# Kernel tuning notes

Hardware: AMD Instinct MI355X
Metric: run time of the kernel (lower is better)

Reference implementation:

```python
import math
import jax, jax.numpy as jnp
from jax import lax
import numpy as np

B, SEQ, D_MODEL = 8, 1024, 512
R, K, H = 3, 3, 4
DE, DH, DU, DTR, DCONV, DEMB = 64, 64, 32, 4, 3, 10


def setup_inputs() -> dict:
    key = jax.random.key(0)
    ks = iter(jax.random.split(key, 48))
    def nrm(shape, s=0.05):
        return jax.random.normal(next(ks), shape, jnp.float32) * s
    inp = {}
    inp['x'] = jax.random.normal(next(ks), (B, SEQ, D_MODEL), jnp.float32)
    # Mamba params, leading dims (R, 2) = (layer, fwd/bwd direction)
    inp['m_in_w'] = nrm((R, 2, D_MODEL, 2 * DE))
    inp['m_conv_w'] = nrm((R, 2, DE, DCONV), 0.2)
    inp['m_conv_b'] = nrm((R, 2, DE), 0.1)
    inp['m_xproj_w'] = nrm((R, 2, DE, DTR + 2 * DH))
    inp['m_dt_w'] = nrm((R, 2, DTR, DE), 0.2)
    inp['m_dt_b'] = nrm((R, 2, DE), 0.1)
    inp['m_Alog'] = jnp.broadcast_to(jnp.log(jnp.arange(1, DH + 1, dtype=jnp.float32)), (R, 2, DE, DH)) + jnp.zeros((R, 2, DE, DH), jnp.float32)
    inp['m_D'] = jnp.ones((R, 2, DE), jnp.float32)
    inp['m_out_w'] = nrm((R, 2, DE, D_MODEL))
    # LayerNorm / FFN params per layer
    inp['ln1_g'] = jnp.ones((R, D_MODEL), jnp.float32)
    inp['ln1_b'] = jnp.zeros((R, D_MODEL), jnp.float32)
    inp['ffn_w1'] = nrm((R, D_MODEL, DU))
    inp['ffn_b1'] = jnp.zeros((R, DU), jnp.float32)
    inp['ffn_w2'] = nrm((R, DU, D_MODEL))
    inp['ffn_b2'] = jnp.zeros((R, D_MODEL), jnp.float32)
    inp['ln2_g'] = jnp.ones((R, D_MODEL), jnp.float32)
    inp['ln2_b'] = jnp.zeros((R, D_MODEL), jnp.float32)
    # MAGAC params (N = D_MODEL nodes, in_dim = SEQ)
    inp['psi_emb'] = jax.random.normal(next(ks), (D_MODEL, DEMB), jnp.float32)
    inp['psi'] = jnp.array(1.0, jnp.float32)
    inp['W_q'] = jax.random.normal(next(ks), (DEMB, H, DEMB), jnp.float32)
    inp['W_k'] = jax.random.normal(next(ks), (DEMB, H, DEMB), jnp.float32)
    inp['attn_alpha'] = jnp.array(0.5, jnp.float32)
    inp['F_w'] = nrm((H, DEMB, K + 1, SEQ))
    inp['f_b'] = jax.random.normal(next(ks), (H, DEMB), jnp.float32)
    inp['head_mix'] = jnp.ones((H,), jnp.float32)
    inp['head_w'] = nrm((D_MODEL,))
    inp['head_b'] = jnp.zeros((), jnp.float32)
    return inp


def _layernorm(x, g, b, eps=1e-5):
    mu = x.mean(-1, keepdims=True)
    v = ((x - mu) ** 2).mean(-1, keepdims=True)
    return (x - mu) / jnp.sqrt(v + eps) * g + b


def _mamba(x, in_w, conv_w, conv_b, xproj_w, dt_w, dt_b, Alog, Dp, out_w):
    b, l, _ = x.shape
    xr = x @ in_w                              # (b,l,2*DE)
    xp, res = jnp.split(xr, 2, axis=-1)
    # depthwise causal conv (torch pads k-1 both sides then truncates to l == left-pad k-1)
    xc = xp.transpose(0, 2, 1)                 # (b,DE,l)
    xc = lax.conv_general_dilated(xc, conv_w[:, None, :], (1,), [(DCONV - 1, 0)],
                                  feature_group_count=DE,
                                  dimension_numbers=('NCH', 'OIH', 'NCH'))
    xc = xc + conv_b[None, :, None]
    xp = jax.nn.silu(xc.transpose(0, 2, 1))    # (b,l,DE)
    A = -jnp.exp(Alog)                         # (DE,DH)
    x_dbl = xp @ xproj_w                       # (b,l,DTR+2*DH)
    delta = jax.nn.softplus(x_dbl[..., :DTR] @ dt_w + dt_b)   # (b,l,DE)
    Bm = x_dbl[..., DTR:DTR + DH]
    Cm = x_dbl[..., DTR + DH:]
    dA = jnp.exp(delta[..., None] * A)                         # (b,l,DE,DH)
    dBu = delta[..., None] * Bm[:, :, None, :] * xp[..., None] # (b,l,DE,DH)
    def step(s, inp):
        dAt, dBt, ct = inp
        s = dAt * s + dBt
        return s, jnp.einsum('bdn,bn->bd', s, ct)
    s0 = jnp.zeros((b, DE, DH), x.dtype)
    _, ys = lax.scan(step, s0, (dA.transpose(1, 0, 2, 3), dBu.transpose(1, 0, 2, 3), Cm.transpose(1, 0, 2)))
    y = ys.transpose(1, 0, 2) + xp * Dp
    y = y * jax.nn.sigmoid(res)
    return y @ out_w


def _magac(xg, psi_emb, psi, W_q, W_k, attn_alpha, F_w, f_b, head_mix):
    # xg: (B, N, L); eval-mode deterministic path
    diff = psi_emb[:, None, :] - psi_emb[None, :, :]
    A_base = jax.nn.softmax(jnp.exp(-psi * (diff ** 2).sum(-1)), axis=1)   # (N,N)
    Q = jnp.einsum('nd,dhm->nhm', psi_emb, W_q)
    Kq = jnp.einsum('nd,dhm->nhm', psi_emb, W_k)
    attn = jax.nn.softmax(jnp.einsum('nhd,mhd->hnm', Q, Kq) / math.sqrt(DEMB), axis=-1)
    alpha = jax.nn.sigmoid(attn_alpha)
    A_eff = alpha * A_base[None] + (1.0 - alpha) * attn                    # (H,N,N)
    N = psi_emb.shape[0]
    I = jnp.broadcast_to(jnp.eye(N, dtype=xg.dtype), (H, N, N))
    sup = [I, A_eff]
    for _ in range(K - 1):
        sup.append(2.0 * jnp.matmul(A_eff, sup[-1]) - sup[-2])             # Chebyshev
    sup = jnp.stack(sup, axis=1)                                           # (H,K+1,N,N)
    Wf = jnp.einsum('nd,hdkl->hnkl', psi_emb, F_w)                         # (H,N,K+1,L)
    bf = jnp.einsum('nd,hd->hn', psi_emb, f_b)                             # (H,N)
    x_g = jnp.einsum('hknm,bml->bhknl', sup, xg)                           # (B,H,K+1,N,L)
    out_h = jnp.einsum('bhknl,hnkl->bhn', x_g, Wf) + bf[None]
    mix = jax.nn.softmax(head_mix)
    return jnp.einsum('bhn,h->bn', out_h, mix)


def reference(x, m_in_w, m_conv_w, m_conv_b, m_xproj_w, m_dt_w, m_dt_b, m_Alog, m_D, m_out_w,
              ln1_g, ln1_b, ffn_w1, ffn_b1, ffn_w2, ffn_b2, ln2_g, ln2_b,
              psi_emb, psi, W_q, W_k, attn_alpha, F_w, f_b, head_mix, head_w, head_b):
    for i in range(R):
        mf = (m_in_w[i, 0], m_conv_w[i, 0], m_conv_b[i, 0], m_xproj_w[i, 0], m_dt_w[i, 0],
              m_dt_b[i, 0], m_Alog[i, 0], m_D[i, 0], m_out_w[i, 0])
        mb = (m_in_w[i, 1], m_conv_w[i, 1], m_conv_b[i, 1], m_xproj_w[i, 1], m_dt_w[i, 1],
              m_dt_b[i, 1], m_Alog[i, 1], m_D[i, 1], m_out_w[i, 1])
        y_f = _mamba(x, *mf)
        y_b = jnp.flip(_mamba(jnp.flip(x, 1), *mb), 1)
        y = _layernorm(x + y_f + y_b, ln1_g[i], ln1_b[i])
        z = jax.nn.relu(y @ ffn_w1[i] + ffn_b1[i]) @ ffn_w2[i] + ffn_b2[i]
        x = _layernorm(y + z, ln2_g[i], ln2_b[i])
    g = _magac(x.transpose(0, 2, 1), psi_emb, psi, W_q, W_k, attn_alpha, F_w, f_b, head_mix)
    # eval-mode Bayesian MC: all mc_eval samples identical -> mean=g, var=1e-6
    log_var_node = jnp.full_like(g, jnp.log(jnp.asarray(1e-6, g.dtype)))
    mu = g @ head_w + head_b
    var = jnp.exp(log_var_node) @ (head_w ** 2) + 1e-6
    return mu, jnp.log(var)
```

## Files before the change

### kernel.cpp

```cpp
#include <hip/hip_runtime.h>
#include <math.h>

#define SEQL 1024
#define NB 8
#define DMOD 512

__device__ __forceinline__ float blk_sum4(float v, volatile float* sb) {
#pragma unroll
  for (int off = 32; off; off >>= 1) v += __shfl_xor(v, off, 64);
  int lid = threadIdx.x & 63, wid = threadIdx.x >> 6;
  if (lid == 0) sb[wid] = v;
  __syncthreads();
  float t = sb[0] + sb[1] + sb[2] + sb[3];
  __syncthreads();
  return t;
}
__device__ __forceinline__ float blk_max4(float v, volatile float* sb) {
#pragma unroll
  for (int off = 32; off; off >>= 1) v = fmaxf(v, __shfl_xor(v, off, 64));
  int lid = threadIdx.x & 63, wid = threadIdx.x >> 6;
  if (lid == 0) sb[wid] = v;
  __syncthreads();
  float t = fmaxf(fmaxf(sb[0], sb[1]), fmaxf(sb[2], sb[3]));
  __syncthreads();
  return t;
}

__global__ __launch_bounds__(256) void gemm_f32(
    const float* __restrict__ A, long aStr,
    const float* __restrict__ B, long bStr,
    const float* __restrict__ Dm, long dStr,
    float* __restrict__ C, long cStr, long cChunkStr,
    int M, int N, int K, int lda, int ldb, int ldd, int ldc,
    float alpha, float beta, int kchunks) {
  __shared__ float As[2][16][68];
  __shared__ float Bs[2][16][64];
  const int zz = blockIdx.z;
  const int zb = zz / kchunks, kc = zz % kchunks;
  A += (long)zb * aStr + (long)kc * K;
  B += (long)zb * bStr + (long)kc * K * ldb;
  Dm += (long)zb * dStr;
  C += (long)zb * cStr + (long)kc * cChunkStr;
  const int tid = threadIdx.x;
  const int m0 = blockIdx.y * 64, n0 = blockIdx.x * 64;
  const int tx = tid & 15, ty = tid >> 4;
  const int arow = tid >> 2, acol = (tid & 3) << 2;
  const int brow = tid >> 4, bcol = (tid & 15) << 2;
  const bool aOk = (m0 + arow < M);
  const float* Aptr = A + (long)(m0 + arow) * lda + acol;
  const float* Bptr = B + (long)brow * ldb;
  const int bc = n0 + bcol;
  const int kIters = K >> 4;
  float acc[4][4] = {};

  auto loadB = [&](int it) {
    const float* Bk = Bptr + (long)it * 16 * ldb;
    float4 r;
    if (bc + 3 < N) r = *(const float4*)(Bk + bc);
    else {
      r.x = (bc + 0 < N) ? Bk[bc + 0] : 0.f;
      r.y = (bc + 1 < N) ? Bk[bc + 1] : 0.f;
      r.z = (bc + 2 < N) ? Bk[bc + 2] : 0.f;
      r.w = (bc + 3 < N) ? Bk[bc + 3] : 0.f;
    }
    return r;
  };

  float4 av = make_float4(0.f, 0.f, 0.f, 0.f);
  if (aOk) av = *(const float4*)(Aptr);
  float4 bv = loadB(0);
  As[0][acol + 0][arow] = av.x; As[0][acol + 1][arow] = av.y;
  As[0][acol + 2][arow] = av.z; As[0][acol + 3][arow] = av.w;
  *(float4*)&Bs[0][brow][bcol] = bv;

  for (int it = 0; it < kIters; ++it) {
    const int cur = it & 1;
    __syncthreads();
    const bool more = (it + 1 < kIters);
    if (more) {
      if (aOk) av = *(const float4*)(Aptr + (it + 1) * 16);
      bv = loadB(it + 1);
    }
#pragma unroll
    for (int kk = 0; kk < 16; ++kk) {
      float4 aq = *(const float4*)&As[cur][kk][ty << 2];
      float4 bq = *(const float4*)&Bs[cur][kk][tx << 2];
      float aa[4] = {aq.x, aq.y, aq.z, aq.w};
      float bb[4] = {bq.x, bq.y, bq.z, bq.w};
#pragma unroll
      for (int i = 0; i < 4; ++i)
#pragma unroll
        for (int j = 0; j < 4; ++j) acc[i][j] = fmaf(aa[i], bb[j], acc[i][j]);
    }
    if (more) {
      const int nxt = cur ^ 1;
      As[nxt][acol + 0][arow] = av.x; As[nxt][acol + 1][arow] = av.y;
      As[nxt][acol + 2][arow] = av.z; As[nxt][acol + 3][arow] = av.w;
      *(float4*)&Bs[nxt][brow][bcol] = bv;
    }
  }
#pragma unroll
  for (int i = 0; i < 4; ++i) {
    int row = m0 + (ty << 2) + i;
    if (row >= M) continue;
#pragma unroll
    for (int j = 0; j < 4; ++j) {
      int col = n0 + (tx << 2) + j;
      if (col >= N) continue;
      float v = alpha * acc[i][j];
      if (beta != 0.f) v += beta * Dm[(long)row * ldd + col];
      C[(long)row * ldc + col] = v;
    }
  }
}

__global__ __launch_bounds__(256) void conv_silu(
    const float* __restrict__ xr, float* __restrict__ xp,
    const float* __restrict__ cw, const float* __restrict__ cb) {
  int dir = blockIdx.y;
  int idx = blockIdx.x * 256 + threadIdx.x;
  const float* xrp = xr + (long)dir * 1048576;
  float* xpp = xp + (long)dir * 524288;
  const float* w = cw + dir * 192;
  int e = idx & 63;
  int t = (idx >> 6) & 1023;
  long rb = (long)(idx >> 6) * 128;
  float w0 = w[e * 3 + 0], w1 = w[e * 3 + 1], w2 = w[e * 3 + 2];
  float acc = cb[dir * 64 + e] + w2 * xrp[rb + e];
  if (dir == 0) {
    if (t >= 1) acc += w1 * xrp[rb - 128 + e];
    if (t >= 2) acc += w0 * xrp[rb - 256 + e];
  } else {
    if (t <= 1022) acc += w1 * xrp[rb + 128 + e];
    if (t <= 1021) acc += w0 * xrp[rb + 256 + e];
  }
  xpp[idx] = acc / (1.f + __expf(-acc));
}

__global__ __launch_bounds__(64) void proj_kernel(
    const float* __restrict__ xp, const float* __restrict__ pw,
    const float* __restrict__ dw, const float* __restrict__ db,
    float* __restrict__ dl, float* __restrict__ Bm, float* __restrict__ Cm) {
  int tok = blockIdx.x, dir = blockIdx.y, j = threadIdx.x;
  const float* xpp = xp + (long)dir * 524288 + (long)tok * 64;
  const float* w = pw + dir * 8448;
  __shared__ float xs[64];
  __shared__ float dpre[4];
  xs[j] = xpp[j];
  __syncthreads();
  float aB = 0.f, aC = 0.f, aD = 0.f;
  for (int k = 0; k < 64; ++k) {
    float xv = xs[k];
    const float* wr = w + k * 132;
    aB = fmaf(xv, wr[4 + j], aB);
    aC = fmaf(xv, wr[68 + j], aC);
    aD = fmaf(xv, wr[j & 3], aD);
  }
  long ob = (long)dir * 524288 + (long)tok * 64;
  Bm[ob + j] = aB;
  Cm[ob + j] = aC;
  if (j < 4) dpre[j] = aD;
  __syncthreads();
  const float* dwp = dw + dir * 256;
  float dv = db[dir * 64 + j];
#pragma unroll
  for (int r = 0; r < 4; ++r) dv = fmaf(dpre[r], dwp[r * 64 + j], dv);
  dl[ob + j] = fmaxf(dv, 0.f) + log1pf(__expf(-fabsf(dv)));
}

__device__ __forceinline__ void scan_remap(int& d, int& b, int& dir, int& c) {
  int L = blockIdx.x + 64 * (blockIdx.y + 8 * blockIdx.z);
  int r = L & 7, q = L >> 3;
  d = q & 63;
  int T = (q >> 6) * 8 + r;
  b = T >> 5;
  dir = (T >> 4) & 1;
  c = T & 15;
}

__global__ __launch_bounds__(64) void scan_p1(
    const float* __restrict__ dl, const float* __restrict__ Bm,
    const float* __restrict__ xp, const float* __restrict__ Alog,
    float* __restrict__ Aprod, float* __restrict__ Send) {
  int d, b, dir, c;
  scan_remap(d, b, dir, c);
  int n = threadIdx.x;
  long doff = (long)dir * 524288;
  int tln = c * 64 + n;
  int tgn = dir ? 1023 - tln : tln;
  float dlv_v = dl[doff + ((long)b * 1024 + tgn) * 64 + d];
  float xpv_v = xp[doff + ((long)b * 1024 + tgn) * 64 + d];
  float a_dn = -__expf(Alog[dir * 4096 + d * 64 + n]);
  int t0 = c * 64;
  int tg0 = dir ? (1023 - t0) : t0;
  long bstride = dir ? -64 : 64;
  const float* bp = Bm + doff + ((long)b * 1024 + tg0) * 64 + n;
  float s = 0.f, ap = 1.f;
#pragma unroll 8
  for (int st = 0; st < 64; ++st) {
    float bt = *bp; bp += bstride;
    float dlv = __shfl(dlv_v, st);
    float xpv = __shfl(xpv_v, st);
    float a = __expf(dlv * a_dn);
    ap *= a;
    s = fmaf(a, s, (dlv * xpv) * bt);
  }
  long sidx = ((long)((dir * 8 + b) * 64 + d)) * 1024 + c * 64 + n;
  Aprod[sidx] = ap;
  Send[sidx] = s;
}

__global__ __launch_bounds__(64) void scan_p2(
    const float* __restrict__ Aprod, const float* __restrict__ Send,
    float* __restrict__ Sin) {
  int d = blockIdx.x, b = blockIdx.y, dir = blockIdx.z;
  int n = threadIdx.x;
  long base = ((long)((dir * 8 + b) * 64 + d)) * 1024;
  float s = 0.f;
#pragma unroll
  for (int c = 0; c < 16; ++c) {
    Sin[base + c * 64 + n] = s;
    s = fmaf(Aprod[base + c * 64 + n], s, Send[base + c * 64 + n]);
  }
}

__global__ __launch_bounds__(64) void scan_p3(
    const float* __restrict__ dl, const float* __restrict__ Bm,
    const float* __restrict__ Cm, const float* __restrict__ xp,
    const float* __restrict__ xr, const float* __restrict__ Alog,
    const float* __restrict__ Dp, const float* __restrict__ Sin,
    float* __restrict__ ycat) {
  __shared__ float sP[16 * 65];
  int d, b, dir, c;
  scan_remap(d, b, dir, c);
  int n = threadIdx.x;
  long doff = (long)dir * 524288;
  int tln = c * 64 + n;
  int tgn = dir ? 1023 - tln : tln;
  float dlv_v = dl[doff + ((long)b * 1024 + tgn) * 64 + d];
  float xpv_v = xp[doff + ((long)b * 1024 + tgn) * 64 + d];
  float a_dn = -__expf(Alog[dir * 4096 + d * 64 + n]);
  float dpd = Dp[dir * 64 + d];
  int t0 = c * 64;
  int tg0 = dir ? (1023 - t0) : t0;
  long bstride = dir ? -64 : 64;
  const float* bp = Bm + doff + ((long)b * 1024 + tg0) * 64 + n;
  const float* cp = Cm + doff + ((long)b * 1024 + tg0) * 64 + n;
  const float* xrp = xr + (long)dir * 1048576 + (long)b * 131072;
  long sidx = ((long)((dir * 8 + b) * 64 + d)) * 1024 + c * 64 + n;
  float s = Sin[sidx];
  int r4 = n >> 2, q4 = n & 3;
  for (int sb = 0; sb < 4; ++sb) {
#pragma unroll
    for (int k = 0; k < 16; ++k) {
      int st = sb * 16 + k;
      float bt = *bp; bp += bstride;
      float ct = *cp; cp += bstride;
      float dlv = __shfl(dlv_v, st);
      float xpv = __shfl(xpv_v, st);
      float a = __expf(dlv * a_dn);
      s = fmaf(a, s, (dlv * xpv) * bt);
      sP[k * 65 + n] = s * ct;
    }
    __syncthreads();
    float p = 0.f;
#pragma unroll
    for (int k = 0; k < 16; ++k) p += sP[r4 * 65 + q4 * 16 + k];
    p += __shfl_xor(p, 1, 64);
    p += __shfl_xor(p, 2, 64);
    float xpv_r = __shfl(xpv_v, sb * 16 + r4);
    if (q4 == 0) {
      int tl = c * 64 + sb * 16 + r4;
      int tg = dir ? 1023 - tl : tl;
      float rres = xrp[(long)tg * 128 + 64 + d];
      ycat[((long)b * 1024 + tg) * 128 + dir * 64 + d] =
          (p + xpv_r * dpd) * (1.f / (1.f + __expf(-rres)));
    }
    __syncthreads();
  }
}

__global__ __launch_bounds__(256) void ln_ffn_ln(
    float* __restrict__ x, const float* __restrict__ g1, const float* __restrict__ b1v,
    const float* __restrict__ w1, const float* __restrict__ bb1,
    const float* __restrict__ w2, const float* __restrict__ bb2,
    const float* __restrict__ g2, const float* __restrict__ b2v) {
  __shared__ float ybuf[2][512];
  __shared__ float rbuf[2][256];
  __shared__ float zbuf[2][32];
  __shared__ float red4[16];
  int tid = threadIdx.x;
  int lid = tid & 63, wid = tid >> 6;
  float* row0 = x + (long)blockIdx.x * 1024;
  float* row1 = row0 + 512;
  float a0 = row0[tid], b0 = row0[tid + 256];
  float a1 = row1[tid], b1 = row1[tid + 256];
  float s0 = a0 + b0, q0 = a0 * a0 + b0 * b0;
  float s1 = a1 + b1, q1 = a1 * a1 + b1 * b1;
#pragma unroll
  for (int off = 32; off; off >>= 1) {
    s0 += __shfl_xor(s0, off, 64); q0 += __shfl_xor(q0, off, 64);
    s1 += __shfl_xor(s1, off, 64); q1 += __shfl_xor(q1, off, 64);
  }
  if (lid == 0) {
    red4[wid * 4 + 0] = s0; red4[wid * 4 + 1] = q0;
    red4[wid * 4 + 2] = s1; red4[wid * 4 + 3] = q1;
  }
  __syncthreads();
  float S0 = red4[0] + red4[4] + red4[8] + red4[12];
  float Q0 = red4[1] + red4[5] + red4[9] + red4[13];
  float S1 = red4[2] + red4[6] + red4[10] + red4[14];
  float Q1 = red4[3] + red4[7] + red4[11] + red4[15];
  float mu0 = S0 * (1.f / 512.f), mu1 = S1 * (1.f / 512.f);
  float r0 = 1.f / sqrtf(Q0 * (1.f / 512.f) - mu0 * mu0 + 1e-5f);
  float r1 = 1.f / sqrtf(Q1 * (1.f / 512.f) - mu1 * mu1 + 1e-5f);
  float g1a = g1[tid], g1b = g1[tid + 256];
  float b1a = b1v[tid], b1b = b1v[tid + 256];
  float y0a = (a0 - mu0) * r0 * g1a + b1a;
  float y0b = (b0 - mu0) * r0 * g1b + b1b;
  float y1a = (a1 - mu1) * r1 * g1a + b1a;
  float y1b = (b1 - mu1) * r1 * g1b + b1b;
  ybuf[0][tid] = y0a; ybuf[0][tid + 256] = y0b;
  ybuf[1][tid] = y1a; ybuf[1][tid + 256] = y1b;
  __syncthreads();
  int u = tid & 31, seg = tid >> 5;
  int k0 = seg * 64;
  float p0 = 0.f, p1 = 0.f;
#pragma unroll
  for (int k = 0; k < 64; k += 4) {
    float4 ya = *(const float4*)&ybuf[0][k0 + k];
    float4 yb = *(const float4*)&ybuf[1][k0 + k];
    float w1v0 = w1[(k0 + k + 0) * 32 + u];
    float w1v1 = w1[(k0 + k + 1) * 32 + u];
    float w1v2 = w1[(k0 + k + 2) * 32 + u];
    float w1v3 = w1[(k0 + k + 3) * 32 + u];
    p0 = fmaf(ya.w, w1v3, fmaf(ya.z, w1v2, fmaf(ya.y, w1v1, fmaf(ya.x, w1v0, p0))));
    p1 = fmaf(yb.w, w1v3, fmaf(yb.z, w1v2, fmaf(yb.y, w1v1, fmaf(yb.x, w1v0, p1))));
  }
  rbuf[0][seg * 32 + u] = p0;
  rbuf[1][seg * 32 + u] = p1;
  __syncthreads();
  if (tid < 64) {
    int t = tid >> 5, uu = tid & 31;
    float zv = bb1[uu];
#pragma unroll
    for (int sg = 0; sg < 8; ++sg) zv += rbuf[t][sg * 32 + uu];
    zbuf[t][uu] = fmaxf(zv, 0.f);
  }
  __syncthreads();
  float bb2a = bb2[tid], bb2b = bb2[tid + 256];
  float h0a = y0a + bb2a, h0b = y0b + bb2b;
  float h1a = y1a + bb2a, h1b = y1b + bb2b;
#pragma unroll
  for (int uu = 0; uu < 32; ++uu) {
    float wa = w2[uu * 512 + tid], wb = w2[uu * 512 + tid + 256];
    float z0 = zbuf[0][uu], z1 = zbuf[1][uu];
    h0a = fmaf(z0, wa, h0a); h1a = fmaf(z1, wa, h1a);
    h0b = fmaf(z0, wb, h0b); h1b = fmaf(z1, wb, h1b);
  }
  s0 = h0a + h0b; q0 = h0a * h0a + h0b * h0b;
  s1 = h1a + h1b; q1 = h1a * h1a + h1b * h1b;
#pragma unroll
  for (int off = 32; off; off >>= 1) {
    s0 += __shfl_xor(s0, off, 64); q0 += __shfl_xor(q0, off, 64);
    s1 += __shfl_xor(s1, off, 64); q1 += __shfl_xor(q1, off, 64);
  }
  __syncthreads();
  if (lid == 0) {
    red4[wid * 4 + 0] = s0; red4[wid * 4 + 1] = q0;
    red4[wid * 4 + 2] = s1; red4[wid * 4 + 3] = q1;
  }
  __syncthreads();
  S0 = red4[0] + red4[4] + red4[8] + red4[12];
  Q0 = red4[1] + red4[5] + red4[9] + red4[13];
  S1 = red4[2] + red4[6] + red4[10] + red4[14];
  Q1 = red4[3] + red4[7] + red4[11] + red4[15];
  mu0 = S0 * (1.f / 512.f); mu1 = S1 * (1.f / 512.f);
  r0 = 1.f / sqrtf(Q0 * (1.f / 512.f) - mu0 * mu0 + 1e-5f);
  r1 = 1.f / sqrtf(Q1 * (1.f / 512.f) - mu1 * mu1 + 1e-5f);
  float g2a = g2[tid], g2b = g2[tid + 256];
  float b2a = b2v[tid], b2b = b2v[tid + 256];
  row0[tid] = (h0a - mu0) * r0 * g2a + b2a;
  row0[tid + 256] = (h0b - mu0) * r0 * g2b + b2b;
  row1[tid] = (h1a - mu1) * r1 * g2a + b2a;
  row1[tid + 256] = (h1b - mu1) * r1 * g2b + b2b;
}

__global__ __launch_bounds__(64) void qk_kernel(
    const float* __restrict__ e, const float* __restrict__ Wq,
    const float* __restrict__ Wk, float* __restrict__ Qb, float* __restrict__ Kb) {
  int n = blockIdx.x, j = threadIdx.x;
  __shared__ float en[10];
  if (j < 10) en[j] = e[n * 10 + j];
  __syncthreads();
  if (j < 40) {
    float q = 0.f, k = 0.f;
#pragma unroll
    for (int dd = 0; dd < 10; ++dd) {
      q = fmaf(en[dd], Wq[dd * 40 + j], q);
      k = fmaf(en[dd], Wk[dd * 40 + j], k);
    }
    Qb[n * 40 + j] = q;
    Kb[n * 40 + j] = k;
  }
}

__global__ __launch_bounds__(256) void aeff_kernel(
    const float* __restrict__ e, const float* __restrict__ Qb,
    const float* __restrict__ Kb, const float* __restrict__ psi_p,
    const float* __restrict__ alpha_p, float* __restrict__ Aef) {
  int n = blockIdx.x, h = blockIdx.y, tid = threadIdx.x;
  __shared__ float s_at[512];
  __shared__ float s_bs[512];
  __shared__ float qn[10];
  __shared__ float en[10];
  __shared__ float red[4];
  if (tid < 10) { qn[tid] = Qb[n * 40 + h * 10 + tid]; en[tid] = e[n * 10 + tid]; }
  __syncthreads();
  float psi = psi_p[0];
  float alpha = 1.f / (1.f + __expf(-alpha_p[0]));
  const float isq = 0.3162277660168379f;
  for (int m = tid; m < 512; m += 256) {
    float sc = 0.f, d2 = 0.f;
#pragma unroll
    for (int dd = 0; dd < 10; ++dd) {
      sc = fmaf(qn[dd], Kb[m * 40 + h * 10 + dd], sc);
      float df = en[dd] - e[m * 10 + dd];
      d2 = fmaf(df, df, d2);
    }
    s_at[m] = sc * isq;
    s_bs[m] = __expf(-psi * d2);
  }
  __syncthreads();
  float m1 = -1e30f, m2 = -1e30f;
  for (int m = tid; m < 512; m += 256) { m1 = fmaxf(m1, s_at[m]); m2 = fmaxf(m2, s_bs[m]); }
  m1 = blk_max4(m1, red);
  m2 = blk_max4(m2, red);
  float e1 = 0.f, e2 = 0.f;
  for (int m = tid; m < 512; m += 256) {
    float a = __expf(s_at[m] - m1); s_at[m] = a; e1 += a;
    float bq = __expf(s_bs[m] - m2); s_bs[m] = bq; e2 += bq;
  }
  e1 = blk_sum4(e1, red);
  e2 = blk_sum4(e2, red);
  float r1 = (1.f - alpha) / e1, r2 = alpha / e2;
  float* outp = Aef + (long)h * 262144 + (long)n * 512;
  for (int m = tid; m < 512; m += 256) outp[m] = r2 * s_bs[m] + r1 * s_at[m];
}

__global__ void xpose_kernel(const float* __restrict__ DbufP,
                             float* __restrict__ X3, float* __restrict__ X2s,
                             float* __restrict__ X13, float* __restrict__ X02) {
  int idx = blockIdx.x * 256 + threadIdx.x;
  if (idx >= 163840) return;
  int c = idx % 80;
  int m = (idx / 80) % 512;
  int h = idx / 40960;
  int d = c >> 3, b = c & 7;
  long base = (long)(b * 160 + h * 40 + d * 4) * 512 + m;
  float k0 = 0.f, k1 = 0.f, k2 = 0.f, k3 = 0.f;
#pragma unroll
  for (int p = 0; p < 4; ++p) {
    const float* Dp_ = DbufP + (long)p * 655360;
    k0 += Dp_[base];
    k1 += Dp_[base + 512];
    k2 += Dp_[base + 1024];
    k3 += Dp_[base + 1536];
  }
  X3[idx] = k3;
  X2s[idx] = k2;
  X13[idx] = k1 - 3.f * k3;
  X02[idx] = k0 - k2;
}

__global__ void outh_kernel(const float* __restrict__ e, const float* __restrict__ fb,
                            const float* __restrict__ Zt, const float* __restrict__ hm,
                            float* __restrict__ g) {
  int idx = blockIdx.x * 256 + threadIdx.x;
  if (idx >= 4096) return;
  int n = idx & 511, b = idx >> 9;
  float h0 = hm[0], h1 = hm[1], h2 = hm[2], h3 = hm[3];
  float mx = fmaxf(fmaxf(h0, h1), fmaxf(h2, h3));
  float x0 = __expf(h0 - mx), x1 = __expf(h1 - mx), x2 = __expf(h2 - mx), x3 = __expf(h3 - mx);
  float es = x0 + x1 + x2 + x3;
  float mixv[4] = {x0 / es, x1 / es, x2 / es, x3 / es};
  float acc = 0.f;
  for (int h = 0; h < 4; ++h) {
    float oh = 0.f;
#pragma unroll
    for (int dd = 0; dd < 10; ++dd) {
      float ev = e[n * 10 + dd];
      float v = Zt[((long)h * 512 + n) * 80 + dd * 8 + b] + fb[h * 10 + dd];
      oh = fmaf(ev, v, oh);
    }
    acc = fmaf(mixv[h], oh, acc);
  }
  g[b * 512 + n] = acc;
}

__global__ __launch_bounds__(256) void head_kernel(
    const float* __restrict__ g, const float* __restrict__ hw,
    const float* __restrict__ hb, float* __restrict__ out) {
  __shared__ float red[4];
  int b = blockIdx.x, tid = threadIdx.x;
  float w0 = hw[tid], w1 = hw[tid + 256];
  float v = g[b * 512 + tid] * w0 + g[b * 512 + tid + 256] * w1;
  float q = w0 * w0 + w1 * w1;
  float mu = blk_sum4(v, red);
  float s2 = blk_sum4(q, red);
  if (tid == 0) {
    out[b] = mu + hb[0];
    out[8 + b] = logf(1e-6f * s2 + 1e-6f);
  }
}

extern "C" void kernel_launch(void* const* d_in, const int* in_sizes, int n_in,
                              void* d_out, int out_size, void* d_ws, size_t ws_size,
                              hipStream_t stream) {
  (void)in_sizes; (void)n_in; (void)out_size; (void)ws_size;
  const float* x0    = (const float*)d_in[0];
  const float* in_w  = (const float*)d_in[1];
  const float* cw    = (const float*)d_in[2];
  const float* cb    = (const float*)d_in[3];
  const float* pw    = (const float*)d_in[4];
  const float* dtw   = (const float*)d_in[5];
  const float* dtb   = (const float*)d_in[6];
  const float* Alog  = (const float*)d_in[7];
  const float* Dpar  = (const float*)d_in[8];
  const float* ow    = (const float*)d_in[9];
  const float* l1g   = (const float*)d_in[10];
  const float* l1b   = (const float*)d_in[11];
  const float* fw1   = (const float*)d_in[12];
  const float* fb1   = (const float*)d_in[13];
  const float* fw2   = (const float*)d_in[14];
  const float* fb2   = (const float*)d_in[15];
  const float* l2g   = (const float*)d_in[16];
  const float* l2b   = (const float*)d_in[17];
  const float* emb   = (const float*)d_in[18];
  const float* psi   = (const float*)d_in[19];
  const float* Wq    = (const float*)d_in[20];
  const float* Wk    = (const float*)d_in[21];
  const float* aal   = (const float*)d_in[22];
  const float* Fw    = (const float*)d_in[23];
  const float* fbv   = (const float*)d_in[24];
  const float* hmix  = (const float*)d_in[25];
  const float* hw    = (const float*)d_in[26];
  const float* hb    = (const float*)d_in[27];
  float* out = (float*)d_out;

  float* ws = (float*)d_ws;
  float* xA   = ws;
  float* xB   = xA + 4194304;
  float* scr  = xB + 4194304;
  float* xr   = scr;
  float* xp   = xr + 2097152;
  float* dl   = xp + 1048576;
  float* Bm   = dl + 1048576;
  float* Cm   = Bm + 1048576;
  float* ycat = Cm + 1048576;
  float* Aprod = scr + 7340032;
  float* Send  = Aprod + 1048576;
  float* Sin   = Send + 1048576;
  float* Qb    = scr;
  float* Kb    = Qb + 20480;
  float* Aef   = Kb + 20480;
  float* DbufP = Aef + 1048576;
  float* X3    = DbufP + 2621440;
  float* X2s   = X3 + 163840;
  float* X13   = X2s + 163840;
  float* X02   = X13 + 163840;
  float* Z2    = X02 + 163840;
  float* Z1    = Z2 + 163840;
  float* Zt    = Z1 + 163840;
  float* gb    = Zt + 163840;

  const float* xin = x0;
  float* bufs[3] = {xA, xB, xA};
  for (int i = 0; i < 3; ++i) {
    float* xout = bufs[i];
    gemm_f32<<<dim3(2, 128, 2), 256, 0, stream>>>(
        xin, 0, in_w + (long)i * 131072, 65536, xin, 0, xr, 1048576, 0,
        8192, 128, 512, 512, 128, 0, 128, 1.f, 0.f, 1);
    conv_silu<<<dim3(2048, 2), 256, 0, stream>>>(xr, xp, cw + i * 384, cb + i * 128);
    proj_kernel<<<dim3(8192, 2), 64, 0, stream>>>(
        xp, pw + i * 16896, dtw + i * 512, dtb + i * 128, dl, Bm, Cm);
    scan_p1<<<dim3(64, 8, 32), 64, 0, stream>>>(
        dl, Bm, xp, Alog + i * 8192, Aprod, Send);
    scan_p2<<<dim3(64, 8, 2), 64, 0, stream>>>(Aprod, Send, Sin);
    scan_p3<<<dim3(64, 8, 32), 64, 0, stream>>>(
        dl, Bm, Cm, xp, xr, Alog + i * 8192, Dpar + i * 128, Sin, ycat);
    gemm_f32<<<dim3(8, 128, 1), 256, 0, stream>>>(
        ycat, 0, ow + (long)i * 65536, 0, xin, 0, xout, 0, 0,
        8192, 512, 128, 128, 512, 512, 512, 1.f, 1.f, 1);
    ln_ffn_ln<<<4096, 256, 0, stream>>>(
        xout, l1g + i * 512, l1b + i * 512, fw1 + i * 16384, fb1 + i * 32,
        fw2 + i * 16384, fb2 + i * 512, l2g + i * 512, l2b + i * 512);
    xin = xout;
  }
  qk_kernel<<<512, 64, 0, stream>>>(emb, Wq, Wk, Qb, Kb);
  aeff_kernel<<<dim3(512, 4), 256, 0, stream>>>(emb, Qb, Kb, psi, aal, Aef);
  gemm_f32<<<dim3(8, 3, 32), 256, 0, stream>>>(
      Fw, 0, xA, 524288, Fw, 0, DbufP, 81920, 655360,
      160, 512, 256, 1024, 512, 0, 512, 1.f, 0.f, 4);
  xpose_kernel<<<640, 256, 0, stream>>>(DbufP, X3, X2s, X13, X02);
  gemm_f32<<<dim3(2, 8, 4), 256, 0, stream>>>(
      Aef, 262144, X3, 40960, X2s, 40960, Z2, 40960, 0,
      512, 80, 512, 512, 80, 80, 80, 4.f, 2.f, 1);
  gemm_f32<<<dim3(2, 8, 4), 256, 0, stream>>>(
      Aef, 262144, Z2, 40960, X13, 40960, Z1, 40960, 0,
      512, 80, 512, 512, 80, 80, 80, 1.f, 1.f, 1);
  gemm_f32<<<dim3(2, 8, 4), 256, 0, stream>>>(
      Aef, 262144, Z1, 40960, X02, 40960, Zt, 40960, 0,
      512, 80, 512, 512, 80, 80, 80, 1.f, 1.f, 1);
  outh_kernel<<<16, 256, 0, stream>>>(emb, fbv, Zt, hmix, gb);
  head_kernel<<<8, 256, 0, stream>>>(gb, hw, hb, out);
}
```

Measured before the change: 743.6 us.

## Fuse conv and projection, store scan inputs transposed, halve scan chunk count

Merges conv_silu and proj_kernel into one kernel that uses wave shuffles instead of shared memory. The fused kernel also precomputes the sigmoid gate and writes xp, delta and gate in a time-contiguous transposed layout, so the scan kernels get coalesced loads and no longer re-read xr. The scan chunks grow from 64 to 128 steps, halving the number of chunk blocks and the size of the Aprod/Send carry buffers. In exchange the transposed writes from convproj are strided, and the longer sequential chunks lower parallelism in the scan phases.

```diff
diff --git a/kernel.cpp b/kernel.cpp
--- a/kernel.cpp
+++ b/kernel.cpp
@@ -114,17 +114,22 @@
   }
 }
 
-__global__ __launch_bounds__(256) void conv_silu(
-    const float* __restrict__ xr, float* __restrict__ xp,
-    const float* __restrict__ cw, const float* __restrict__ cb) {
+__global__ __launch_bounds__(256) void convproj(
+    const float* __restrict__ xr, const float* __restrict__ cw,
+    const float* __restrict__ cb, const float* __restrict__ pw,
+    const float* __restrict__ dw, const float* __restrict__ db,
+    float* __restrict__ Bm, float* __restrict__ Cm,
+    float* __restrict__ xpT, float* __restrict__ dlT, float* __restrict__ sigT) {
   int dir = blockIdx.y;
-  int idx = blockIdx.x * 256 + threadIdx.x;
+  int L = blockIdx.x;
+  int r = L & 7, q = L >> 3;
+  int blk = r * 256 + q;
+  int wv = threadIdx.x >> 6, e = threadIdx.x & 63;
+  int tok = blk * 4 + wv;
+  int b = tok >> 10, t = tok & 1023;
   const float* xrp = xr + (long)dir * 1048576;
-  float* xpp = xp + (long)dir * 524288;
+  long rb = (long)tok * 128;
   const float* w = cw + dir * 192;
-  int e = idx & 63;
-  int t = (idx >> 6) & 1023;
-  long rb = (long)(idx >> 6) * 128;
   float w0 = w[e * 3 + 0], w1 = w[e * 3 + 1], w2 = w[e * 3 + 2];
   float acc = cb[dir * 64 + e] + w2 * xrp[rb + e];
   if (dir == 0) {
@@ -134,78 +139,77 @@
     if (t <= 1022) acc += w1 * xrp[rb + 128 + e];
     if (t <= 1021) acc += w0 * xrp[rb + 256 + e];
   }
-  xpp[idx] = acc / (1.f + __expf(-acc));
-}
-
-__global__ __launch_bounds__(64) void proj_kernel(
-    const float* __restrict__ xp, const float* __restrict__ pw,
-    const float* __restrict__ dw, const float* __restrict__ db,
-    float* __restrict__ dl, float* __restrict__ Bm, float* __restrict__ Cm) {
-  int tok = blockIdx.x, dir = blockIdx.y, j = threadIdx.x;
-  const float* xpp = xp + (long)dir * 524288 + (long)tok * 64;
-  const float* w = pw + dir * 8448;
-  __shared__ float xs[64];
-  __shared__ float dpre[4];
-  xs[j] = xpp[j];
-  __syncthreads();
+  float xpv = acc / (1.f + __expf(-acc));
+  float res = xrp[rb + 64 + e];
+  float sg = 1.f / (1.f + __expf(-res));
+  long tidx = (long)dir * 524288 + (long)b * 65536 + (long)e * 1024 + t;
+  xpT[tidx] = xpv;
+  sigT[tidx] = sg;
+  const float* wp = pw + dir * 8448;
   float aB = 0.f, aC = 0.f, aD = 0.f;
+#pragma unroll
   for (int k = 0; k < 64; ++k) {
-    float xv = xs[k];
-    const float* wr = w + k * 132;
-    aB = fmaf(xv, wr[4 + j], aB);
-    aC = fmaf(xv, wr[68 + j], aC);
-    aD = fmaf(xv, wr[j & 3], aD);
+    float xk = __shfl(xpv, k, 64);
+    const float* wr = wp + k * 132;
+    aB = fmaf(xk, wr[4 + e], aB);
+    aC = fmaf(xk, wr[68 + e], aC);
+    aD = fmaf(xk, wr[e & 3], aD);
   }
   long ob = (long)dir * 524288 + (long)tok * 64;
-  Bm[ob + j] = aB;
-  Cm[ob + j] = aC;
-  if (j < 4) dpre[j] = aD;
-  __syncthreads();
+  Bm[ob + e] = aB;
+  Cm[ob + e] = aC;
   const float* dwp = dw + dir * 256;
-  float dv = db[dir * 64 + j];
-#pragma unroll
-  for (int r = 0; r < 4; ++r) dv = fmaf(dpre[r], dwp[r * 64 + j], dv);
-  dl[ob + j] = fmaxf(dv, 0.f) + log1pf(__expf(-fabsf(dv)));
-}
-
-__device__ __forceinline__ void scan_remap(int& d, int& b, int& dir, int& c) {
+  float dv = db[dir * 64 + e];
+#pragma unroll
+  for (int rr = 0; rr < 4; ++rr) dv = fmaf(__shfl(aD, rr, 64), dwp[rr * 64 + e], dv);
+  dlT[tidx] = fmaxf(dv, 0.f) + log1pf(__expf(-fabsf(dv)));
+}
+
+__device__ __forceinline__ void remap8(int& d, int& b, int& dir, int& c) {
   int L = blockIdx.x + 64 * (blockIdx.y + 8 * blockIdx.z);
   int r = L & 7, q = L >> 3;
   d = q & 63;
   int T = (q >> 6) * 8 + r;
-  b = T >> 5;
-  dir = (T >> 4) & 1;
-  c = T & 15;
+  b = T >> 4;
+  dir = (T >> 3) & 1;
+  c = T & 7;
 }
 
 __global__ __launch_bounds__(64) void scan_p1(
-    const float* __restrict__ dl, const float* __restrict__ Bm,
-    const float* __restrict__ xp, const float* __restrict__ Alog,
+    const float* __restrict__ dlT, const float* __restrict__ xpT,
+    const float* __restrict__ Bm, const float* __restrict__ Alog,
     float* __restrict__ Aprod, float* __restrict__ Send) {
   int d, b, dir, c;
-  scan_remap(d, b, dir, c);
+  remap8(d, b, dir, c);
   int n = threadIdx.x;
-  long doff = (long)dir * 524288;
-  int tln = c * 64 + n;
-  int tgn = dir ? 1023 - tln : tln;
-  float dlv_v = dl[doff + ((long)b * 1024 + tgn) * 64 + d];
-  float xpv_v = xp[doff + ((long)b * 1024 + tgn) * 64 + d];
+  long tbase = (long)dir * 524288 + (long)b * 65536 + (long)d * 1024;
+  int t0 = c * 128;
+  float dl0, dl1, u0, u1;
+  if (dir == 0) {
+    dl0 = dlT[tbase + t0 + n];       dl1 = dlT[tbase + t0 + 64 + n];
+    u0 = xpT[tbase + t0 + n] * dl0;  u1 = xpT[tbase + t0 + 64 + n] * dl1;
+  } else {
+    dl0 = dlT[tbase + 1023 - t0 - n];      dl1 = dlT[tbase + 959 - t0 - n];
+    u0 = xpT[tbase + 1023 - t0 - n] * dl0; u1 = xpT[tbase + 959 - t0 - n] * dl1;
+  }
   float a_dn = -__expf(Alog[dir * 4096 + d * 64 + n]);
-  int t0 = c * 64;
   int tg0 = dir ? (1023 - t0) : t0;
-  long bstride = dir ? -64 : 64;
-  const float* bp = Bm + doff + ((long)b * 1024 + tg0) * 64 + n;
+  long bstep = dir ? -64 : 64;
+  const float* bp = Bm + (long)dir * 524288 + ((long)b * 1024 + tg0) * 64 + n;
   float s = 0.f, ap = 1.f;
-#pragma unroll 8
-  for (int st = 0; st < 64; ++st) {
-    float bt = *bp; bp += bstride;
-    float dlv = __shfl(dlv_v, st);
-    float xpv = __shfl(xpv_v, st);
-    float a = __expf(dlv * a_dn);
-    ap *= a;
-    s = fmaf(a, s, (dlv * xpv) * bt);
-  }
-  long sidx = ((long)((dir * 8 + b) * 64 + d)) * 1024 + c * 64 + n;
+  for (int h = 0; h < 2; ++h) {
+    float dlh = h ? dl1 : dl0, uh = h ? u1 : u0;
+#pragma unroll
+    for (int st = 0; st < 64; ++st) {
+      float bt = *bp; bp += bstep;
+      float dlv = __shfl(dlh, st, 64);
+      float uu = __shfl(uh, st, 64);
+      float a = __expf(dlv * a_dn);
+      ap *= a;
+      s = fmaf(a, s, uu * bt);
+    }
+  }
+  long sidx = ((long)((dir * 8 + b) * 64 + d)) * 512 + c * 64 + n;
   Aprod[sidx] = ap;
   Send[sidx] = s;
 }
@@ -215,51 +219,60 @@
     float* __restrict__ Sin) {
   int d = blockIdx.x, b = blockIdx.y, dir = blockIdx.z;
   int n = threadIdx.x;
-  long base = ((long)((dir * 8 + b) * 64 + d)) * 1024;
+  long base = ((long)((dir * 8 + b) * 64 + d)) * 512;
   float s = 0.f;
 #pragma unroll
-  for (int c = 0; c < 16; ++c) {
+  for (int c = 0; c < 8; ++c) {
     Sin[base + c * 64 + n] = s;
     s = fmaf(Aprod[base + c * 64 + n], s, Send[base + c * 64 + n]);
   }
 }
 
 __global__ __launch_bounds__(64) void scan_p3(
-    const float* __restrict__ dl, const float* __restrict__ Bm,
-    const float* __restrict__ Cm, const float* __restrict__ xp,
-    const float* __restrict__ xr, const float* __restrict__ Alog,
+    const float* __restrict__ dlT, const float* __restrict__ xpT,
+    const float* __restrict__ sigT, const float* __restrict__ Bm,
+    const float* __restrict__ Cm, const float* __restrict__ Alog,
     const float* __restrict__ Dp, const float* __restrict__ Sin,
     float* __restrict__ ycat) {
   __shared__ float sP[16 * 65];
   int d, b, dir, c;
-  scan_remap(d, b, dir, c);
+  remap8(d, b, dir, c);
   int n = threadIdx.x;
-  long doff = (long)dir * 524288;
-  int tln = c * 64 + n;
-  int tgn = dir ? 1023 - tln : tln;
-  float dlv_v = dl[doff + ((long)b * 1024 + tgn) * 64 + d];
-  float xpv_v = xp[doff + ((long)b * 1024 + tgn) * 64 + d];
+  long tbase = (long)dir * 524288 + (long)b * 65536 + (long)d * 1024;
+  int t0 = c * 128;
+  float dl0, dl1, xp0, xp1, sg0, sg1;
+  if (dir == 0) {
+    dl0 = dlT[tbase + t0 + n];      dl1 = dlT[tbase + t0 + 64 + n];
+    xp0 = xpT[tbase + t0 + n];      xp1 = xpT[tbase + t0 + 64 + n];
+    sg0 = sigT[tbase + t0 + n];     sg1 = sigT[tbase + t0 + 64 + n];
+  } else {
+    dl0 = dlT[tbase + 1023 - t0 - n];  dl1 = dlT[tbase + 959 - t0 - n];
+    xp0 = xpT[tbase + 1023 - t0 - n];  xp1 = xpT[tbase + 959 - t0 - n];
+    sg0 = sigT[tbase + 1023 - t0 - n]; sg1 = sigT[tbase + 959 - t0 - n];
+  }
+  float u0 = xp0 * dl0, u1 = xp1 * dl1;
   float a_dn = -__expf(Alog[dir * 4096 + d * 64 + n]);
   float dpd = Dp[dir * 64 + d];
-  int t0 = c * 64;
   int tg0 = dir ? (1023 - t0) : t0;
-  long bstride = dir ? -64 : 64;
-  const float* bp = Bm + doff + ((long)b * 1024 + tg0) * 64 + n;
-  const float* cp = Cm + doff + ((long)b * 1024 + tg0) * 64 + n;
-  const float* xrp = xr + (long)dir * 1048576 + (long)b * 131072;
-  long sidx = ((long)((dir * 8 + b) * 64 + d)) * 1024 + c * 64 + n;
+  long bstep = dir ? -64 : 64;
+  long boff = (long)dir * 524288 + ((long)b * 1024 + tg0) * 64 + n;
+  const float* bp = Bm + boff;
+  const float* cp = Cm + boff;
+  long sidx = ((long)((dir * 8 + b) * 64 + d)) * 512 + c * 64 + n;
   float s = Sin[sidx];
   int r4 = n >> 2, q4 = n & 3;
-  for (int sb = 0; sb < 4; ++sb) {
+  for (int phase = 0; phase < 8; ++phase) {
+    int h = phase >> 2;
+    float dlh = h ? dl1 : dl0, uh = h ? u1 : u0;
 #pragma unroll
     for (int k = 0; k < 16; ++k) {
-      int st = sb * 16 + k;
-      float bt = *bp; bp += bstride;
-      float ct = *cp; cp += bstride;
-      float dlv = __shfl(dlv_v, st);
-      float xpv = __shfl(xpv_v, st);
+      int st = (phase & 3) * 16 + k;
+      float bt = *bp; bp += bstep;
+      float ct = *cp; cp += bstep;
+      float dlv = __shfl(dlh, st, 64);
+      float uu = __shfl(uh, st, 64);
       float a = __expf(dlv * a_dn);
-      s = fmaf(a, s, (dlv * xpv) * bt);
+      s = fmaf(a, s, uu * bt);
       sP[k * 65 + n] = s * ct;
     }
     __syncthreads();
@@ -268,13 +281,13 @@
     for (int k = 0; k < 16; ++k) p += sP[r4 * 65 + q4 * 16 + k];
     p += __shfl_xor(p, 1, 64);
     p += __shfl_xor(p, 2, 64);
-    float xpv_r = __shfl(xpv_v, sb * 16 + r4);
+    int stl = (phase & 3) * 16 + r4;
+    float xpv_r = __shfl(h ? xp1 : xp0, stl, 64);
+    float sgv = __shfl(h ? sg1 : sg0, stl, 64);
     if (q4 == 0) {
-      int tl = c * 64 + sb * 16 + r4;
+      int tl = t0 + phase * 16 + r4;
       int tg = dir ? 1023 - tl : tl;
-      float rres = xrp[(long)tg * 128 + 64 + d];
-      ycat[((long)b * 1024 + tg) * 128 + dir * 64 + d] =
-          (p + xpv_r * dpd) * (1.f / (1.f + __expf(-rres)));
+      ycat[((long)b * 1024 + tg) * 128 + dir * 64 + d] = (p + xpv_r * dpd) * sgv;
     }
     __syncthreads();
   }
@@ -553,14 +566,15 @@
   float* xB   = xA + 4194304;
   float* scr  = xB + 4194304;
   float* xr   = scr;
-  float* xp   = xr + 2097152;
-  float* dl   = xp + 1048576;
-  float* Bm   = dl + 1048576;
+  float* Bm   = xr + 2097152;
   float* Cm   = Bm + 1048576;
-  float* ycat = Cm + 1048576;
-  float* Aprod = scr + 7340032;
-  float* Send  = Aprod + 1048576;
-  float* Sin   = Send + 1048576;
+  float* xpT  = Cm + 1048576;
+  float* dlT  = xpT + 1048576;
+  float* sigT = dlT + 1048576;
+  float* ycat = sigT + 1048576;
+  float* Aprod = ycat + 1048576;
+  float* Send  = Aprod + 524288;
+  float* Sin   = Send + 524288;
   float* Qb    = scr;
   float* Kb    = Qb + 20480;
   float* Aef   = Kb + 20480;
@@ -581,14 +595,14 @@
     gemm_f32<<<dim3(2, 128, 2), 256, 0, stream>>>(
         xin, 0, in_w + (long)i * 131072, 65536, xin, 0, xr, 1048576, 0,
         8192, 128, 512, 512, 128, 0, 128, 1.f, 0.f, 1);
-    conv_silu<<<dim3(2048, 2), 256, 0, stream>>>(xr, xp, cw + i * 384, cb + i * 128);
-    proj_kernel<<<dim3(8192, 2), 64, 0, stream>>>(
-        xp, pw + i * 16896, dtw + i * 512, dtb + i * 128, dl, Bm, Cm);
-    scan_p1<<<dim3(64, 8, 32), 64, 0, stream>>>(
-        dl, Bm, xp, Alog + i * 8192, Aprod, Send);
+    convproj<<<dim3(2048, 2), 256, 0, stream>>>(
+        xr, cw + i * 384, cb + i * 128, pw + i * 16896, dtw + i * 512,
+        dtb + i * 128, Bm, Cm, xpT, dlT, sigT);
+    scan_p1<<<dim3(64, 8, 16), 64, 0, stream>>>(
+        dlT, xpT, Bm, Alog + i * 8192, Aprod, Send);
     scan_p2<<<dim3(64, 8, 2), 64, 0, stream>>>(Aprod, Send, Sin);
-    scan_p3<<<dim3(64, 8, 32), 64, 0, stream>>>(
-        dl, Bm, Cm, xp, xr, Alog + i * 8192, Dpar + i * 128, Sin, ycat);
+    scan_p3<<<dim3(64, 8, 16), 64, 0, stream>>>(
+        dlT, xpT, sigT, Bm, Cm, Alog + i * 8192, Dpar + i * 128, Sin, ycat);
     gemm_f32<<<dim3(8, 128, 1), 256, 0, stream>>>(
         ycat, 0, ow + (long)i * 65536, 0, xin, 0, xout, 0, 0,
         8192, 512, 128, 128, 512, 512, 512, 1.f, 1.f, 1);
```

Result: slower. 882.0 us (+18.6%).
